# Performance work log

Measured on AMD Instinct MI355X. Metric: run time of the kernel, lower is better.

Reference implementation:

```python
import jax, jax.numpy as jnp
import numpy as np

NUM_WAVELETS = 64      # W
NUM_OUT_CH = 32        # W' (one 2-layer MLP per output channel)
HIDDEN_DIM = 128       # H


def setup_inputs() -> dict:
    key = jax.random.key(0)
    k_x, k_w1, k_b1, k_w2, k_b2 = jax.random.split(key, 5)
    N, C, W, H, O = 4096, 32, NUM_WAVELETS, HIDDEN_DIM, NUM_OUT_CH
    # torch nn.Linear default init: U(-1/sqrt(fan_in), 1/sqrt(fan_in))
    lim1 = 1.0 / np.sqrt(W)
    lim2 = 1.0 / np.sqrt(H)
    return {
        "scalar_inputs": jax.random.normal(k_x, (N, C, W), dtype=jnp.float32),
        # Stacked weights of the O independent MLPs:
        "W1": jax.random.uniform(k_w1, (O, H, W), jnp.float32, -lim1, lim1),
        "b1": jax.random.uniform(k_b1, (O, H), jnp.float32, -lim1, lim1),
        "W2": jax.random.uniform(k_w2, (O, H), jnp.float32, -lim2, lim2),  # Linear(H->1) weight per MLP
        "b2": jax.random.uniform(k_b2, (O,), jnp.float32, -lim2, lim2),
    }


def reference(scalar_inputs, W1, b1, W2, b2):
    # scalar_inputs: [N, C, W]; W1: [O, H, W]; b1: [O, H]; W2: [O, H]; b2: [O]
    N, C, W = scalar_inputs.shape
    x = scalar_inputs.reshape(N * C, W)                      # [NC, W]
    # Batched first Linear over all O MLPs at once (replaces the per-MLP loop)
    h = jax.nn.silu(jnp.einsum("nw,ohw->noh", x, W1) + b1)   # [NC, O, H]
    out = jnp.einsum("noh,oh->no", h, W2) + b2               # [NC, O]
    return out.reshape(N, C, -1)                             # [N, C, O]
```

## Files before the change

kernel.cpp:

```cpp
#include <hip/hip_runtime.h>

#define NC    131072
#define WDIM  64
#define ODIM  32
#define HDIM  128
#define LOG2E 1.4426950408889634f
#define LN2   0.6931471805599453f

typedef __attribute__((ext_vector_type(8))) short bf16x8;
typedef __attribute__((ext_vector_type(4))) float f32x4;
typedef __attribute__((ext_vector_type(4))) float flt4;

__device__ __forceinline__ short f2bf(float f) {
    union { float f; unsigned u; } v; v.f = f;
    unsigned r = (v.u + 0x7FFFu + ((v.u >> 16) & 1u)) >> 16;
    return (short)r;
}

__global__ void prep_kernel(const float* __restrict__ W1, const float* __restrict__ b1,
                            const float* __restrict__ w2, short* __restrict__ w1f,
                            float* __restrict__ b1s, float* __restrict__ w2s) {
    if (blockIdx.x < 128) {
        int tid  = blockIdx.x * 256 + threadIdx.x;
        int lane = tid & 63;
        int frag = (tid >> 6) & 15;
        int o    = tid >> 10;
        int t    = frag >> 1;
        int k2   = frag & 1;
        const float* src = W1 + ((size_t)(o * HDIM + t * 16 + (lane & 15)) * WDIM
                                 + k2 * 32 + (lane >> 4) * 8);
        bf16x8 v;
        #pragma unroll
        for (int i = 0; i < 8; ++i) v[i] = f2bf(src[i] * -LOG2E);
        *reinterpret_cast<bf16x8*>(w1f + (size_t)tid * 8) = v;
    } else if (blockIdx.x < 144) {
        int idx = (blockIdx.x - 128) * 256 + threadIdx.x;
        b1s[idx] = b1[idx] * -LOG2E;
    } else {
        int idx = (blockIdx.x - 144) * 256 + threadIdx.x;
        w2s[idx] = w2[idx] * -LN2;
    }
}

__device__ __forceinline__ void async16(void* lds_dst, const void* g_src) {
    __builtin_amdgcn_global_load_lds(
        (const __attribute__((address_space(1))) unsigned int*)g_src,
        (__attribute__((address_space(3))) unsigned int*)lds_dst,
        16, 0, 0);
}

__global__ __launch_bounds__(256, 4)
void swr_main(const float* __restrict__ x, const short* __restrict__ w1f,
              const float* __restrict__ b1s, const float* __restrict__ w2s,
              const float* __restrict__ b2, float* __restrict__ out)
{
    __shared__ short w1lds[2 * 8192];
    const int tid  = threadIdx.x;
    const int lane = tid & 63;
    const int wid  = tid >> 6;
    const int col  = lane & 15;
    const int kq   = lane >> 4;
    const size_t rowbase = (size_t)blockIdx.x * 128 + (size_t)wid * 32;

    bf16x8 afrag[2][2];
    #pragma unroll
    for (int s = 0; s < 2; ++s) {
        #pragma unroll
        for (int k2 = 0; k2 < 2; ++k2) {
            const float* p = x + (rowbase + s * 16 + col) * WDIM + k2 * 32 + kq * 8;
            flt4 lo = *reinterpret_cast<const flt4*>(p);
            flt4 hi = *reinterpret_cast<const flt4*>(p + 4);
            bf16x8 a;
            a[0] = f2bf(lo[0]); a[1] = f2bf(lo[1]); a[2] = f2bf(lo[2]); a[3] = f2bf(lo[3]);
            a[4] = f2bf(hi[0]); a[5] = f2bf(hi[1]); a[6] = f2bf(hi[2]); a[7] = f2bf(hi[3]);
            afrag[s][k2] = a;
        }
    }

    {
        #pragma unroll
        for (int f = 0; f < 4; ++f) {
            int frag = wid * 4 + f;
            async16(&w1lds[frag * 512], w1f + frag * 512 + lane * 8);
        }
    }
    __syncthreads();

    for (int o = 0; o < ODIM; ++o) {
        const short* cur = &w1lds[(o & 1) * 8192];
        if (o + 1 < ODIM) {
            const short* g = w1f + (size_t)(o + 1) * 8192;
            short* nb = &w1lds[((o + 1) & 1) * 8192];
            #pragma unroll
            for (int f = 0; f < 4; ++f) {
                int frag = wid * 4 + f;
                async16(nb + frag * 512, g + frag * 512 + lane * 8);
            }
        }

        float b1v[8], w2v[8];
        #pragma unroll
        for (int t = 0; t < 8; ++t) {
            b1v[t] = b1s[o * HDIM + t * 16 + col];
            w2v[t] = w2s[o * HDIM + t * 16 + col];
        }
        const float b2o = b2[o];

        float part[2][4];
        #pragma unroll
        for (int s = 0; s < 2; ++s)
            #pragma unroll
            for (int r = 0; r < 4; ++r) part[s][r] = 0.f;

        #pragma unroll
        for (int t = 0; t < 8; ++t) {
            bf16x8 bf0 = *reinterpret_cast<const bf16x8*>(cur + (t * 2 + 0) * 512 + lane * 8);
            bf16x8 bf1 = *reinterpret_cast<const bf16x8*>(cur + (t * 2 + 1) * 512 + lane * 8);
            #pragma unroll
            for (int s = 0; s < 2; ++s) {
                f32x4 acc = { b1v[t], b1v[t], b1v[t], b1v[t] };
                acc = __builtin_amdgcn_mfma_f32_16x16x32_bf16(afrag[s][0], bf0, acc, 0, 0, 0);
                acc = __builtin_amdgcn_mfma_f32_16x16x32_bf16(afrag[s][1], bf1, acc, 0, 0, 0);
                #pragma unroll
                for (int r = 0; r < 4; ++r) {
                    float m  = acc[r];
                    float e  = __builtin_amdgcn_exp2f(m);
                    float sg = __builtin_amdgcn_rcpf(1.0f + e);
                    part[s][r] = __builtin_fmaf(m * sg, w2v[t], part[s][r]);
                }
            }
        }

        #pragma unroll
        for (int s = 0; s < 2; ++s) {
            float v[4];
            #pragma unroll
            for (int r = 0; r < 4; ++r) {
                float u = part[s][r];
                u += __shfl_xor(u, 1);
                u += __shfl_xor(u, 2);
                u += __shfl_xor(u, 4);
                u += __shfl_xor(u, 8);
                v[r] = u;
            }
            float sel = (lane & 1) ? ((lane & 2) ? v[3] : v[1])
                                   : ((lane & 2) ? v[2] : v[0]);
            if ((lane & 12) == 0) {
                int rowis = kq * 4 + (lane & 3);
                out[(rowbase + s * 16 + rowis) * ODIM + o] = sel + b2o;
            }
        }
        __syncthreads();
    }
}

extern "C" void kernel_launch(void* const* d_in, const int* in_sizes, int n_in,
                              void* d_out, int out_size, void* d_ws, size_t ws_size,
                              hipStream_t stream)
{
    const float* x  = (const float*)d_in[0];
    const float* W1 = (const float*)d_in[1];
    const float* b1 = (const float*)d_in[2];
    const float* w2 = (const float*)d_in[3];
    const float* b2 = (const float*)d_in[4];
    float* out = (float*)d_out;
    short* w1f = (short*)d_ws;
    float* b1s = (float*)((char*)d_ws + 512 * 1024);
    float* w2s = (float*)((char*)d_ws + 528 * 1024);

    hipLaunchKernelGGL(prep_kernel, dim3(160), dim3(256), 0, stream,
                       W1, b1, w2, w1f, b1s, w2s);
    hipLaunchKernelGGL(swr_main, dim3(NC / 128), dim3(256), 0, stream,
                       x, w1f, b1s, w2s, b2, out);
}
```

Measured before the change: 237.3 us.

## Swap MFMA operands, drop LDS staging, use single-wave blocks with register prefetch

The MFMA operands are swapped so weights become the A operand and activations the B operand. Each lane then holds four hidden units for one row, which replaces the per-row shuffle-and-select reduction with a local sum plus two cross-quad shuffles. Weights are no longer double-buffered in LDS with block barriers. Each single-wave block reads weight fragments straight from global/L2 into registers, prefetching one step ahead. This removes LDS traffic and __syncthreads, at the cost of every wave re-reading the full weight set from cache and a 4x larger grid.

```diff
diff --git a/kernel.cpp b/kernel.cpp
--- a/kernel.cpp
+++ b/kernel.cpp
@@ -42,27 +42,17 @@
     }
 }
 
-__device__ __forceinline__ void async16(void* lds_dst, const void* g_src) {
-    __builtin_amdgcn_global_load_lds(
-        (const __attribute__((address_space(1))) unsigned int*)g_src,
-        (__attribute__((address_space(3))) unsigned int*)lds_dst,
-        16, 0, 0);
-}
-
-__global__ __launch_bounds__(256, 4)
+__global__ __launch_bounds__(64, 6)
 void swr_main(const float* __restrict__ x, const short* __restrict__ w1f,
               const float* __restrict__ b1s, const float* __restrict__ w2s,
               const float* __restrict__ b2, float* __restrict__ out)
 {
-    __shared__ short w1lds[2 * 8192];
-    const int tid  = threadIdx.x;
-    const int lane = tid & 63;
-    const int wid  = tid >> 6;
+    const int lane = threadIdx.x & 63;
     const int col  = lane & 15;
     const int kq   = lane >> 4;
-    const size_t rowbase = (size_t)blockIdx.x * 128 + (size_t)wid * 32;
+    const size_t rowbase = (size_t)blockIdx.x * 32;
 
-    bf16x8 afrag[2][2];
+    bf16x8 xf[2][2];
     #pragma unroll
     for (int s = 0; s < 2; ++s) {
         #pragma unroll
@@ -73,39 +63,22 @@
             bf16x8 a;
             a[0] = f2bf(lo[0]); a[1] = f2bf(lo[1]); a[2] = f2bf(lo[2]); a[3] = f2bf(lo[3]);
             a[4] = f2bf(hi[0]); a[5] = f2bf(hi[1]); a[6] = f2bf(hi[2]); a[7] = f2bf(hi[3]);
-            afrag[s][k2] = a;
+            xf[s][k2] = a;
         }
     }
 
-    {
-        #pragma unroll
-        for (int f = 0; f < 4; ++f) {
-            int frag = wid * 4 + f;
-            async16(&w1lds[frag * 512], w1f + frag * 512 + lane * 8);
-        }
-    }
-    __syncthreads();
+    const bf16x8* wfv = reinterpret_cast<const bf16x8*>(w1f);
+    const flt4*  b1v  = reinterpret_cast<const flt4*>(b1s);
+    const flt4*  w2v  = reinterpret_cast<const flt4*>(w2s);
 
+    bf16x8 f0 = wfv[lane];
+    bf16x8 f1 = wfv[64 + lane];
+    flt4  b1c = b1v[kq];
+    flt4  w2c = w2v[kq];
+
+    #pragma unroll 1
     for (int o = 0; o < ODIM; ++o) {
-        const short* cur = &w1lds[(o & 1) * 8192];
-        if (o + 1 < ODIM) {
-            const short* g = w1f + (size_t)(o + 1) * 8192;
-            short* nb = &w1lds[((o + 1) & 1) * 8192];
-            #pragma unroll
-            for (int f = 0; f < 4; ++f) {
-                int frag = wid * 4 + f;
-                async16(nb + frag * 512, g + frag * 512 + lane * 8);
-            }
-        }
-
-        float b1v[8], w2v[8];
-        #pragma unroll
-        for (int t = 0; t < 8; ++t) {
-            b1v[t] = b1s[o * HDIM + t * 16 + col];
-            w2v[t] = w2s[o * HDIM + t * 16 + col];
-        }
         const float b2o = b2[o];
-
         float part[2][4];
         #pragma unroll
         for (int s = 0; s < 2; ++s)
@@ -114,43 +87,39 @@
 
         #pragma unroll
         for (int t = 0; t < 8; ++t) {
-            bf16x8 bf0 = *reinterpret_cast<const bf16x8*>(cur + (t * 2 + 0) * 512 + lane * 8);
-            bf16x8 bf1 = *reinterpret_cast<const bf16x8*>(cur + (t * 2 + 1) * 512 + lane * 8);
+            int ni = o * 8 + t + 1;
+            if (ni > 255) ni = 255;
+            int fo = ni >> 3, ft = ni & 7;
+            int fb = (fo * 16 + ft * 2) * 64;
+            bf16x8 f0n = wfv[fb + lane];
+            bf16x8 f1n = wfv[fb + 64 + lane];
+            flt4  b1n  = b1v[fo * 32 + ft * 4 + kq];
+            flt4  w2n  = w2v[fo * 32 + ft * 4 + kq];
+
             #pragma unroll
             for (int s = 0; s < 2; ++s) {
-                f32x4 acc = { b1v[t], b1v[t], b1v[t], b1v[t] };
-                acc = __builtin_amdgcn_mfma_f32_16x16x32_bf16(afrag[s][0], bf0, acc, 0, 0, 0);
-                acc = __builtin_amdgcn_mfma_f32_16x16x32_bf16(afrag[s][1], bf1, acc, 0, 0, 0);
+                f32x4 acc = { b1c[0], b1c[1], b1c[2], b1c[3] };
+                acc = __builtin_amdgcn_mfma_f32_16x16x32_bf16(f0, xf[s][0], acc, 0, 0, 0);
+                acc = __builtin_amdgcn_mfma_f32_16x16x32_bf16(f1, xf[s][1], acc, 0, 0, 0);
                 #pragma unroll
                 for (int r = 0; r < 4; ++r) {
                     float m  = acc[r];
                     float e  = __builtin_amdgcn_exp2f(m);
                     float sg = __builtin_amdgcn_rcpf(1.0f + e);
-                    part[s][r] = __builtin_fmaf(m * sg, w2v[t], part[s][r]);
+                    part[s][r] = __builtin_fmaf(m * sg, w2c[r], part[s][r]);
                 }
             }
+            f0 = f0n; f1 = f1n; b1c = b1n; w2c = w2n;
         }
 
         #pragma unroll
         for (int s = 0; s < 2; ++s) {
-            float v[4];
-            #pragma unroll
-            for (int r = 0; r < 4; ++r) {
-                float u = part[s][r];
-                u += __shfl_xor(u, 1);
-                u += __shfl_xor(u, 2);
-                u += __shfl_xor(u, 4);
-                u += __shfl_xor(u, 8);
-                v[r] = u;
-            }
-            float sel = (lane & 1) ? ((lane & 2) ? v[3] : v[1])
-                                   : ((lane & 2) ? v[2] : v[0]);
-            if ((lane & 12) == 0) {
-                int rowis = kq * 4 + (lane & 3);
-                out[(rowbase + s * 16 + rowis) * ODIM + o] = sel + b2o;
-            }
+            float u = (part[s][0] + part[s][1]) + (part[s][2] + part[s][3]);
+            u += __shfl_xor(u, 16);
+            u += __shfl_xor(u, 32);
+            if (lane < 16)
+                out[(rowbase + s * 16 + lane) * ODIM + o] = u + b2o;
         }
-        __syncthreads();
     }
 }
 
@@ -170,6 +139,6 @@
 
     hipLaunchKernelGGL(prep_kernel, dim3(160), dim3(256), 0, stream,
                        W1, b1, w2, w1f, b1s, w2s);
-    hipLaunchKernelGGL(swr_main, dim3(NC / 128), dim3(256), 0, stream,
+    hipLaunchKernelGGL(swr_main, dim3(NC / 32), dim3(64), 0, stream,
                        x, w1f, b1s, w2s, b2, out);
 }
```

Result: slower. 597.5 us (+151.8%).

## Swap MFMA operands so hidden dim lies in rows, use packed-float epilogue

Applied to the files above, without the earlier changes.

Transposes the MFMA product by passing the weight fragment as A and the input rows as B, so each lane's four accumulator entries cover four hidden units of one row. Bias and output weights then load as float4 vectors per t, and the H-reduction becomes mostly in-register plus two cross-lane shuffles instead of four shuffles per accumulator entry. The silu-weight math is written with 2-wide float vectors so the compiler can emit packed FMA/mul. The outer loop is forced not to unroll to limit code size and register pressure.

```diff
diff --git a/kernel.cpp b/kernel.cpp
--- a/kernel.cpp
+++ b/kernel.cpp
@@ -10,6 +10,7 @@
 typedef __attribute__((ext_vector_type(8))) short bf16x8;
 typedef __attribute__((ext_vector_type(4))) float f32x4;
 typedef __attribute__((ext_vector_type(4))) float flt4;
+typedef __attribute__((ext_vector_type(2))) float f32x2;
 
 __device__ __forceinline__ short f2bf(float f) {
     union { float f; unsigned u; } v; v.f = f;
@@ -62,7 +63,7 @@
     const int kq   = lane >> 4;
     const size_t rowbase = (size_t)blockIdx.x * 128 + (size_t)wid * 32;
 
-    bf16x8 afrag[2][2];
+    bf16x8 xf[2][2];
     #pragma unroll
     for (int s = 0; s < 2; ++s) {
         #pragma unroll
@@ -73,19 +74,21 @@
             bf16x8 a;
             a[0] = f2bf(lo[0]); a[1] = f2bf(lo[1]); a[2] = f2bf(lo[2]); a[3] = f2bf(lo[3]);
             a[4] = f2bf(hi[0]); a[5] = f2bf(hi[1]); a[6] = f2bf(hi[2]); a[7] = f2bf(hi[3]);
-            afrag[s][k2] = a;
+            xf[s][k2] = a;
         }
     }
 
-    {
-        #pragma unroll
-        for (int f = 0; f < 4; ++f) {
-            int frag = wid * 4 + f;
-            async16(&w1lds[frag * 512], w1f + frag * 512 + lane * 8);
-        }
+    #pragma unroll
+    for (int f = 0; f < 4; ++f) {
+        int frag = wid * 4 + f;
+        async16(&w1lds[frag * 512], w1f + frag * 512 + lane * 8);
     }
     __syncthreads();
 
+    const flt4* b1v = reinterpret_cast<const flt4*>(b1s);
+    const flt4* w2v = reinterpret_cast<const flt4*>(w2s);
+
+    #pragma unroll 1
     for (int o = 0; o < ODIM; ++o) {
         const short* cur = &w1lds[(o & 1) * 8192];
         if (o + 1 < ODIM) {
@@ -97,58 +100,48 @@
                 async16(nb + frag * 512, g + frag * 512 + lane * 8);
             }
         }
-
-        float b1v[8], w2v[8];
-        #pragma unroll
-        for (int t = 0; t < 8; ++t) {
-            b1v[t] = b1s[o * HDIM + t * 16 + col];
-            w2v[t] = w2s[o * HDIM + t * 16 + col];
-        }
         const float b2o = b2[o];
 
-        float part[2][4];
+        f32x2 part[2][2];
         #pragma unroll
         for (int s = 0; s < 2; ++s)
             #pragma unroll
-            for (int r = 0; r < 4; ++r) part[s][r] = 0.f;
+            for (int p = 0; p < 2; ++p) part[s][p] = (f32x2){0.f, 0.f};
 
         #pragma unroll
         for (int t = 0; t < 8; ++t) {
-            bf16x8 bf0 = *reinterpret_cast<const bf16x8*>(cur + (t * 2 + 0) * 512 + lane * 8);
-            bf16x8 bf1 = *reinterpret_cast<const bf16x8*>(cur + (t * 2 + 1) * 512 + lane * 8);
+            flt4 b1c = b1v[o * 32 + t * 4 + kq];
+            flt4 w2c = w2v[o * 32 + t * 4 + kq];
+            bf16x8 f0 = *reinterpret_cast<const bf16x8*>(cur + (t * 2 + 0) * 512 + lane * 8);
+            bf16x8 f1 = *reinterpret_cast<const bf16x8*>(cur + (t * 2 + 1) * 512 + lane * 8);
             #pragma unroll
             for (int s = 0; s < 2; ++s) {
-                f32x4 acc = { b1v[t], b1v[t], b1v[t], b1v[t] };
-                acc = __builtin_amdgcn_mfma_f32_16x16x32_bf16(afrag[s][0], bf0, acc, 0, 0, 0);
-                acc = __builtin_amdgcn_mfma_f32_16x16x32_bf16(afrag[s][1], bf1, acc, 0, 0, 0);
+                f32x4 acc = __builtin_amdgcn_mfma_f32_16x16x32_bf16(
+                                f0, xf[s][0], (f32x4){b1c[0], b1c[1], b1c[2], b1c[3]}, 0, 0, 0);
+                acc = __builtin_amdgcn_mfma_f32_16x16x32_bf16(f1, xf[s][1], acc, 0, 0, 0);
                 #pragma unroll
-                for (int r = 0; r < 4; ++r) {
-                    float m  = acc[r];
-                    float e  = __builtin_amdgcn_exp2f(m);
-                    float sg = __builtin_amdgcn_rcpf(1.0f + e);
-                    part[s][r] = __builtin_fmaf(m * sg, w2v[t], part[s][r]);
+                for (int p = 0; p < 2; ++p) {
+                    f32x2 m  = { acc[2 * p], acc[2 * p + 1] };
+                    f32x2 wp = { w2c[2 * p], w2c[2 * p + 1] };
+                    f32x2 mw = m * wp;
+                    f32x2 e  = { __builtin_amdgcn_exp2f(m.x),
+                                 __builtin_amdgcn_exp2f(m.y) };
+                    f32x2 d  = e + (f32x2){1.f, 1.f};
+                    f32x2 sg = { __builtin_amdgcn_rcpf(d.x),
+                                 __builtin_amdgcn_rcpf(d.y) };
+                    part[s][p] = __builtin_elementwise_fma(mw, sg, part[s][p]);
                 }
             }
         }
 
         #pragma unroll
         for (int s = 0; s < 2; ++s) {
-            float v[4];
-            #pragma unroll
-            for (int r = 0; r < 4; ++r) {
-                float u = part[s][r];
-                u += __shfl_xor(u, 1);
-                u += __shfl_xor(u, 2);
-                u += __shfl_xor(u, 4);
-                u += __shfl_xor(u, 8);
-                v[r] = u;
-            }
-            float sel = (lane & 1) ? ((lane & 2) ? v[3] : v[1])
-                                   : ((lane & 2) ? v[2] : v[0]);
-            if ((lane & 12) == 0) {
-                int rowis = kq * 4 + (lane & 3);
-                out[(rowbase + s * 16 + rowis) * ODIM + o] = sel + b2o;
-            }
+            f32x2 u2 = part[s][0] + part[s][1];
+            float u = u2.x + u2.y;
+            u += __shfl_xor(u, 16);
+            u += __shfl_xor(u, 32);
+            if (lane < 16)
+                out[(rowbase + s * 16 + lane) * ODIM + o] = u + b2o;
         }
         __syncthreads();
     }
```

Measured after the change: 221.0 us. 6.9% less time.
